# Performance work log

Measured on AMD Instinct MI355X. Metric: run time of the kernel, lower is better.

The kernel has to match this reference:

```python
import jax, jax.numpy as jnp
import numpy as np

K_F = 3
NUM = K_F * K_F - 1          # 8 non-center neighbors
IDX_REF = NUM // 2           # 4 (center insertion index)
PROP_TIME = 18
AFFINITY_GAMMA = 0.5
B, H, W = 4, 480, 640


def _bilinear(img, y, x):
    """Bilinear sample img [H,W] at float coords y,x [K,H,W]; zero outside."""
    Hh, Ww = img.shape
    y0 = jnp.floor(y)
    x0 = jnp.floor(x)

    def gather(yy, xx):
        valid = (yy >= 0) & (yy < Hh) & (xx >= 0) & (xx < Ww)
        yi = jnp.clip(yy.astype(jnp.int32), 0, Hh - 1)
        xi = jnp.clip(xx.astype(jnp.int32), 0, Ww - 1)
        return jnp.where(valid, img[yi, xi], 0.0)

    wy = y - y0
    wx = x - x0
    return ((1 - wy) * (1 - wx) * gather(y0, x0)
            + (1 - wy) * wx * gather(y0, x0 + 1)
            + wy * (1 - wx) * gather(y0 + 1, x0)
            + wy * wx * gather(y0 + 1, x0 + 1))


def _deform_prop(feat, dy, dx, aff):
    """Modulated deformable 3x3 conv with all-ones weight, zero bias, ch=1.
    feat [B,1,H,W]; dy,dx,aff [B,9,H,W]. Output = sum_k aff_k * sample_k."""
    b, _, h, w = feat.shape
    ky = jnp.array([-1, -1, -1, 0, 0, 0, 1, 1, 1], feat.dtype)
    kx = jnp.array([-1, 0, 1, -1, 0, 1, -1, 0, 1], feat.dtype)
    gy = jnp.arange(h, dtype=feat.dtype)[:, None]   # [H,1]
    gx = jnp.arange(w, dtype=feat.dtype)[None, :]   # [1,W]
    py = gy[None, None] + ky[None, :, None, None] + dy  # [B,9,H,W]
    px = gx[None, None] + kx[None, :, None, None] + dx
    samp = jax.vmap(_bilinear)(feat[:, 0], py, px)      # [B,9,H,W]
    return jnp.sum(samp * aff, axis=1, keepdims=True)


def _affinity_normalization(aff, scale):
    # TGASS: tanh / (gamma*num), abs-sum normalize (clamped at 1), reference = 1 - sum
    aff = jnp.tanh(aff) / (scale + 1e-8)
    s = jnp.sum(jnp.abs(aff), axis=1, keepdims=True) + 1e-4
    s = jnp.maximum(s, 1.0)
    aff = aff / s
    aff_ref = 1.0 - jnp.sum(aff, axis=1, keepdims=True)
    return jnp.concatenate([aff[:, :IDX_REF], aff_ref, aff[:, IDX_REF:]], axis=1)


def setup_inputs() -> dict:
    key = jax.random.key(0)
    k1, k2, k3, k4, k5 = jax.random.split(key, 5)
    feat_init = jax.random.uniform(k1, (B, 1, H, W), jnp.float32) * 10.0
    guidance = jax.random.normal(k2, (B, 24, H, W), jnp.float32)
    confidence = jax.random.uniform(k3, (B, 1, H, W), jnp.float32)
    dense = jax.random.uniform(k4, (B, 1, H, W), jnp.float32) * 10.0
    mask = (jax.random.uniform(k5, (B, 1, H, W)) < 0.05).astype(jnp.float32)
    feat_fix = dense * mask
    aff_scale_const = jnp.full((1,), AFFINITY_GAMMA * NUM, jnp.float32)
    return {"feat_init": feat_init, "guidance": guidance,
            "confidence": confidence, "feat_fix": feat_fix,
            "aff_scale_const": aff_scale_const}


def reference(feat_init, guidance, confidence, feat_fix, aff_scale_const):
    b = feat_init.shape[0]
    h, w = feat_init.shape[2], feat_init.shape[3]
    # offsets: chunk guidance into (o1, o2, aff), interleave, insert zero at center
    o1, o2, aff_g = jnp.split(guidance, 3, axis=1)
    off = jnp.concatenate([o1, o2], axis=1).reshape(b, NUM, 2, h, w)
    zc = jnp.zeros((b, 1, 2, h, w), off.dtype)
    off = jnp.concatenate([off[:, :IDX_REF], zc, off[:, IDX_REF:]], axis=1)
    dy, dx = off[:, :, 0], off[:, :, 1]          # [B,9,H,W]
    aff = _affinity_normalization(aff_g, aff_scale_const)

    # preserve_input: fixed-pixel mask (ch_f == 1)
    mask_fix = (feat_fix > 0.0).astype(feat_init.dtype)
    conf = (1.0 - mask_fix) * confidence + mask_fix
    feat = (1.0 - mask_fix) * feat_init + mask_fix * feat_fix

    def step(f, _):
        f = _deform_prop(f * conf, dy, dx, aff)
        f = (1.0 - mask_fix) * f + mask_fix * feat_fix
        return f, None

    feat, _ = jax.lax.scan(step, feat, None, length=PROP_TIME)
    return feat
```

## Files before the change

kernel.cpp:

```cpp
#include <hip/hip_runtime.h>
#include <hip/hip_fp16.h>
#include <hip/hip_cooperative_groups.h>

namespace cg = cooperative_groups;


#define HH 480
#define WW 640
#define BB 4
#define HWSZ (HH * WW)
#define NPIX (BB * HWSZ)
#define PROP_T 18
#define SLACK 704
#define NTHR 256
#define PXT 5
#define NBLK (NPIX / (NTHR * PXT))

struct f2u { float x, y; };

__device__ __forceinline__ float fast_tanh(float x) {
    x = fminf(fmaxf(x, -15.0f), 15.0f);
    float e = __expf(2.0f * x);
    return __fdividef(e - 1.0f, e + 1.0f);
}

__device__ __forceinline__ float affinities(const float* gb, float inv_scale,
                                            float t[8]) {
    float ssum = 1e-4f;
#pragma unroll
    for (int j = 0; j < 8; ++j) {
        float v = fast_tanh(gb[(16 + j) * HWSZ]) * inv_scale;
        t[j] = v; ssum += fabsf(v);
    }
    ssum = fmaxf(ssum, 1.0f);
    float rs = __fdividef(1.0f, ssum);
    float asum = 0.0f;
#pragma unroll
    for (int j = 0; j < 8; ++j) { t[j] *= rs; asum += t[j]; }
    return 1.0f - asum;
}

__device__ __forceinline__ void make_desc(int y, int x, int k,
                                          float dy, float dx, float ak,
                                          unsigned& pk, unsigned short& akh) {
    float py = (float)(y + k / 3 - 1) + dy;
    float px = (float)(x + k % 3 - 1) + dx;
    float y0f = floorf(py), x0f = floorf(px);
    float wy = py - y0f, wx = px - x0f;
    int y0 = (int)y0f, x0 = (int)x0f;
    if (y0 == -1)                 { ak *= wy;        wy = 1.0f; }
    else if (y0 == HH - 1)        { ak *= 1.0f - wy; wy = 0.0f; }
    else if (y0 < -1 || y0 >= HH) { ak = 0.0f; }
    if (x0 == -1)                 { ak *= wx;        wx = 1.0f; }
    else if (x0 == WW - 1)        { ak *= 1.0f - wx; wx = 0.0f; }
    else if (x0 < -1 || x0 >= WW) { ak = 0.0f; }
    int rel;
    if (ak == 0.0f) {
        rel = 0; wy = 0.0f; wx = 0.0f;
    } else {
        int yc = min(max(y0, -1), HH - 1);
        int xc = min(max(x0, -1), WW - 1);
        rel = (yc - y) * WW + (xc - x);
        rel = min(max(rel, -32767), 32767);
    }
    unsigned uy = (unsigned)(int)(wy * 255.0f + 0.5f);
    unsigned ux = (unsigned)(int)(wx * 255.0f + 0.5f);
    pk  = ((unsigned)(unsigned short)(short)rel << 16) | (uy << 8) | ux;
    akh = __half_as_ushort(__float2half(ak));
}

__device__ __forceinline__ float sample_rel(const float* __restrict__ fp,
                                            unsigned pk, unsigned short akh,
                                            float acc) {
    int rel = (int)(short)(pk >> 16);
    float wy = (float)((pk >> 8) & 0xffu) * (1.0f / 255.0f);
    float wx = (float)(pk & 0xffu) * (1.0f / 255.0f);
    float ak = __half2float(__ushort_as_half(akh));
    const float* p = fp + rel;
    f2u r0 = *reinterpret_cast<const f2u*>(p);
    f2u r1 = *reinterpret_cast<const f2u*>(p + WW);
    float bot = ak * wy;
    float top = ak - bot;
    float omwx = 1.0f - wx;
    acc = fmaf(top * omwx, r0.x, acc);
    acc = fmaf(top * wx,   r0.y, acc);
    acc = fmaf(bot * omwx, r1.x, acc);
    acc = fmaf(bot * wx,   r1.y, acc);
    return acc;
}

__global__ __launch_bounds__(NTHR) void precompute_kernel(
    const float* __restrict__ feat_init,
    const float* __restrict__ guid,
    const float* __restrict__ confidence,
    const float* __restrict__ feat_fix,
    const float* __restrict__ aff_scale,
    float* __restrict__ g0,
    unsigned* __restrict__ pk1Arr,
    unsigned short* __restrict__ akArr,
    unsigned* __restrict__ cfArr,
    float* __restrict__ ffpArr) {
    const int pix = blockIdx.x * NTHR + threadIdx.x;
    const int b = pix / HWSZ;
    const int q = pix - b * HWSZ;
    const int y = q / WW;
    const int x = q - y * WW;
    const float* gb = guid + (size_t)b * 24 * HWSZ + q;

    float ff = feat_fix[pix];
    float m  = (ff > 0.0f) ? 1.0f : 0.0f;
    float km = 1.0f - m;
    float conf = km * confidence[pix] + m;
    float f0   = km * feat_init[pix] + m * ff;
    g0[pix] = f0 * conf;
    ffpArr[pix] = m * ff;

    const float inv_scale = __fdividef(1.0f, aff_scale[0] + 1e-8f);
    float t[8];
    float aref = affinities(gb, inv_scale, t);
    cfArr[pix] = ((unsigned)__half_as_ushort(__float2half(aref)) << 16)
               | (unsigned)__half_as_ushort(__float2half(conf));

    unsigned pk[8];
    unsigned short akh[8];
#pragma unroll
    for (int n = 0; n < 8; ++n) {
        const int k = (n < 4) ? n : (n + 1);
        float dy = gb[(2 * n) * HWSZ];
        float dx = gb[(2 * n + 1) * HWSZ];
        make_desc(y, x, k, dy, dx, t[n], pk[n], akh[n]);
    }
    uint4* pd = reinterpret_cast<uint4*>(pk1Arr) + 2 * pix;
    pd[0] = make_uint4(pk[0], pk[1], pk[2], pk[3]);
    pd[1] = make_uint4(pk[4], pk[5], pk[6], pk[7]);
    uint4 kv;
    kv.x = (unsigned)akh[0] | ((unsigned)akh[1] << 16);
    kv.y = (unsigned)akh[2] | ((unsigned)akh[3] << 16);
    kv.z = (unsigned)akh[4] | ((unsigned)akh[5] << 16);
    kv.w = (unsigned)akh[6] | ((unsigned)akh[7] << 16);
    reinterpret_cast<uint4*>(akArr)[pix] = kv;
}

__global__ __launch_bounds__(NTHR, 4) void persist_kernel(
    const unsigned* __restrict__ pk1Arr,
    const unsigned short* __restrict__ akArr,
    const unsigned* __restrict__ cfArr,
    const float* __restrict__ ffpArr,
    float* __restrict__ fA,
    float* __restrict__ fB,
    float* __restrict__ out)
{
    cg::grid_group grid = cg::this_grid();
    const int base = blockIdx.x * (NTHR * PXT) + threadIdx.x;

    uint4 pka[PXT], pkb[PXT], akv[PXT];
    unsigned cfr[PXT];
    float    ffr[PXT];

#pragma unroll
    for (int i = 0; i < PXT; ++i) {
        const int pix = base + i * NTHR;
        const uint4* pd = reinterpret_cast<const uint4*>(pk1Arr) + 2 * pix;
        pka[i] = pd[0];
        pkb[i] = pd[1];
        akv[i] = reinterpret_cast<const uint4*>(akArr)[pix];
        cfr[i] = cfArr[pix];
        ffr[i] = ffpArr[pix];
    }

#pragma unroll 1
    for (int t = 0; t < PROP_T; ++t) {
        grid.sync();
        const float* fin = (t & 1) ? fB : fA;
        float* fout = (t == PROP_T - 1) ? out : ((t & 1) ? fA : fB);
        const bool last = (t == PROP_T - 1);
#pragma unroll
        for (int i = 0; i < PXT; ++i) {
            const int pix = base + i * NTHR;
            const float* fp = fin + pix;
            unsigned c = cfr[i];
            float aref = __half2float(__ushort_as_half((unsigned short)(c >> 16)));
            float conf = __half2float(__ushort_as_half((unsigned short)(c & 0xffffu)));
            float acc = aref * fp[0];
            uint4 A = pka[i], B = pkb[i], K = akv[i];
            acc = sample_rel(fp, A.x, (unsigned short)(K.x & 0xffffu), acc);
            acc = sample_rel(fp, A.y, (unsigned short)(K.x >> 16),     acc);
            acc = sample_rel(fp, A.z, (unsigned short)(K.y & 0xffffu), acc);
            acc = sample_rel(fp, A.w, (unsigned short)(K.y >> 16),     acc);
            acc = sample_rel(fp, B.x, (unsigned short)(K.z & 0xffffu), acc);
            acc = sample_rel(fp, B.y, (unsigned short)(K.z >> 16),     acc);
            acc = sample_rel(fp, B.z, (unsigned short)(K.w & 0xffffu), acc);
            acc = sample_rel(fp, B.w, (unsigned short)(K.w >> 16),     acc);
            float km = (ffr[i] > 0.0f) ? 0.0f : 1.0f;
            float fnew = fmaf(km, acc, ffr[i]);
            fout[pix] = last ? fnew : conf * fnew;
        }
    }
}

__global__ __launch_bounds__(NTHR) void step_kernel(
    const float* __restrict__ fin,
    float* __restrict__ fout,
    const unsigned* __restrict__ pk1Arr,
    const unsigned short* __restrict__ akArr,
    const unsigned* __restrict__ cfArr,
    const float* __restrict__ ffpArr,
    int last) {
    const int pix = blockIdx.x * NTHR + threadIdx.x;
    const float* fp = fin + pix;
    const uint4* pd = reinterpret_cast<const uint4*>(pk1Arr) + 2 * pix;
    uint4 A = pd[0], B = pd[1];
    uint4 K = reinterpret_cast<const uint4*>(akArr)[pix];
    unsigned c = cfArr[pix];
    float ffv = ffpArr[pix];
    float aref = __half2float(__ushort_as_half((unsigned short)(c >> 16)));
    float conf = __half2float(__ushort_as_half((unsigned short)(c & 0xffffu)));
    float acc = aref * fp[0];
    acc = sample_rel(fp, A.x, (unsigned short)(K.x & 0xffffu), acc);
    acc = sample_rel(fp, A.y, (unsigned short)(K.x >> 16),     acc);
    acc = sample_rel(fp, A.z, (unsigned short)(K.y & 0xffffu), acc);
    acc = sample_rel(fp, A.w, (unsigned short)(K.y >> 16),     acc);
    acc = sample_rel(fp, B.x, (unsigned short)(K.z & 0xffffu), acc);
    acc = sample_rel(fp, B.y, (unsigned short)(K.z >> 16),     acc);
    acc = sample_rel(fp, B.z, (unsigned short)(K.w & 0xffffu), acc);
    acc = sample_rel(fp, B.w, (unsigned short)(K.w >> 16),     acc);
    float km = (ffv > 0.0f) ? 0.0f : 1.0f;
    float fnew = fmaf(km, acc, ffv);
    fout[pix] = last ? fnew : conf * fnew;
}

extern "C" void kernel_launch(void* const* d_in, const int* in_sizes, int n_in,
                              void* d_out, int out_size, void* d_ws, size_t ws_size,
                              hipStream_t stream) {
    const float* feat_init  = (const float*)d_in[0];
    const float* guidance   = (const float*)d_in[1];
    const float* confidence = (const float*)d_in[2];
    const float* feat_fix   = (const float*)d_in[3];
    const float* aff_scale  = (const float*)d_in[4];

    const size_t bufFloats = (size_t)NPIX + 2 * SLACK;
    float* bufA = (float*)d_ws;
    float* bufB = bufA + bufFloats;
    unsigned* pk1Arr = (unsigned*)(bufB + bufFloats);
    unsigned short* akArr = (unsigned short*)(pk1Arr + 8 * (size_t)NPIX);
    unsigned* cfArr = (unsigned*)(akArr + 8 * (size_t)NPIX);
    float* ffpArr = (float*)(cfArr + NPIX);
    float* fA = bufA + SLACK;
    float* fB = bufB + SLACK;
    float* outp = (float*)d_out;

    hipMemsetAsync(bufA, 0, SLACK * sizeof(float), stream);
    hipMemsetAsync(bufA + SLACK + NPIX, 0, SLACK * sizeof(float), stream);
    hipMemsetAsync(bufB, 0, SLACK * sizeof(float), stream);
    hipMemsetAsync(bufB + SLACK + NPIX, 0, SLACK * sizeof(float), stream);

    precompute_kernel<<<NPIX / NTHR, NTHR, 0, stream>>>(
        feat_init, guidance, confidence, feat_fix, aff_scale,
        fA, pk1Arr, akArr, cfArr, ffpArr);

    bool tryCoop = false;
    {
        hipFuncAttributes fa{};
        if (hipFuncGetAttributes(&fa, reinterpret_cast<const void*>(persist_kernel))
                == hipSuccess && fa.localSizeBytes == 0) {
            int occ = 0;
            if (hipOccupancyMaxActiveBlocksPerMultiprocessor(
                    &occ, reinterpret_cast<const void*>(persist_kernel), NTHR, 0)
                    == hipSuccess) {
                int dev = 0, cu = 0;
                hipGetDevice(&dev);
                hipDeviceGetAttribute(&cu, hipDeviceAttributeMultiprocessorCount, dev);
                if ((long)occ * cu >= NBLK) tryCoop = true;
            }
        }
    }
    if (tryCoop) {
        void* args[] = { (void*)&pk1Arr, (void*)&akArr, (void*)&cfArr,
                         (void*)&ffpArr, (void*)&fA, (void*)&fB, (void*)&outp };
        if (hipLaunchCooperativeKernel(reinterpret_cast<void*>(persist_kernel),
                                       dim3(NBLK), dim3(NTHR), args, 0, stream)
                == hipSuccess)
            return;
    }

    for (int t = 0; t < PROP_T; ++t) {
        const float* fin = (t & 1) ? fB : fA;
        float* fout = (t == PROP_T - 1) ? outp : ((t & 1) ? fA : fB);
        step_kernel<<<NPIX / NTHR, NTHR, 0, stream>>>(
            fin, fout, pk1Arr, akArr, cfArr, ffpArr, (t == PROP_T - 1) ? 1 : 0);
    }
}
```

Before: 648.0 us.

## Replace cooperative grid.sync with custom atomic counter barrier in persistent kernel

Drops the cooperative-groups launch and grid.sync in favour of a normal launch plus a hand-rolled global barrier: block thread 0 atomically increments a monotonically growing counter and spins with s_sleep until all blocks have arrived. The barrier now runs only between steps, not before the first one. The separate fixed-value array is packed with the conf/aref word into a uint2 so each pixel needs one fewer load. Sched barriers are also inserted to split the sampling code into scheduling regions. The risk is that a non-cooperative launch does not guarantee all blocks are co-resident, which could deadlock if occupancy is lower than computed.

```diff
diff --git a/kernel.cpp b/kernel.cpp
--- a/kernel.cpp
+++ b/kernel.cpp
@@ -1,8 +1,5 @@
 #include <hip/hip_runtime.h>
 #include <hip/hip_fp16.h>
-#include <hip/hip_cooperative_groups.h>
-
-namespace cg = cooperative_groups;
 
 
 #define HH 480
@@ -98,8 +95,7 @@
     float* __restrict__ g0,
     unsigned* __restrict__ pk1Arr,
     unsigned short* __restrict__ akArr,
-    unsigned* __restrict__ cfArr,
-    float* __restrict__ ffpArr) {
+    uint2* __restrict__ cfArr) {
     const int pix = blockIdx.x * NTHR + threadIdx.x;
     const int b = pix / HWSZ;
     const int q = pix - b * HWSZ;
@@ -113,13 +109,16 @@
     float conf = km * confidence[pix] + m;
     float f0   = km * feat_init[pix] + m * ff;
     g0[pix] = f0 * conf;
-    ffpArr[pix] = m * ff;
 
     const float inv_scale = __fdividef(1.0f, aff_scale[0] + 1e-8f);
     float t[8];
     float aref = affinities(gb, inv_scale, t);
-    cfArr[pix] = ((unsigned)__half_as_ushort(__float2half(aref)) << 16)
-               | (unsigned)__half_as_ushort(__float2half(conf));
+    uint2 cf;
+    cf.x = ((unsigned)__half_as_ushort(__float2half(aref)) << 16)
+         | (unsigned)__half_as_ushort(__float2half(conf));
+    float mff = m * ff;
+    cf.y = __float_as_uint(mff);
+    cfArr[pix] = cf;
 
     unsigned pk[8];
     unsigned short akh[8];
@@ -144,18 +143,16 @@
 __global__ __launch_bounds__(NTHR, 4) void persist_kernel(
     const unsigned* __restrict__ pk1Arr,
     const unsigned short* __restrict__ akArr,
-    const unsigned* __restrict__ cfArr,
-    const float* __restrict__ ffpArr,
+    const uint2* __restrict__ cfArr,
     float* __restrict__ fA,
     float* __restrict__ fB,
-    float* __restrict__ out)
+    float* __restrict__ out,
+    int* __restrict__ bar)
 {
-    cg::grid_group grid = cg::this_grid();
     const int base = blockIdx.x * (NTHR * PXT) + threadIdx.x;
 
     uint4 pka[PXT], pkb[PXT], akv[PXT];
-    unsigned cfr[PXT];
-    float    ffr[PXT];
+    uint2 cfr[PXT];
 
 #pragma unroll
     for (int i = 0; i < PXT; ++i) {
@@ -165,12 +162,10 @@
         pkb[i] = pd[1];
         akv[i] = reinterpret_cast<const uint4*>(akArr)[pix];
         cfr[i] = cfArr[pix];
-        ffr[i] = ffpArr[pix];
     }
 
 #pragma unroll 1
     for (int t = 0; t < PROP_T; ++t) {
-        grid.sync();
         const float* fin = (t & 1) ? fB : fA;
         float* fout = (t == PROP_T - 1) ? out : ((t & 1) ? fA : fB);
         const bool last = (t == PROP_T - 1);
@@ -178,7 +173,7 @@
         for (int i = 0; i < PXT; ++i) {
             const int pix = base + i * NTHR;
             const float* fp = fin + pix;
-            unsigned c = cfr[i];
+            unsigned c = cfr[i].x;
             float aref = __half2float(__ushort_as_half((unsigned short)(c >> 16)));
             float conf = __half2float(__ushort_as_half((unsigned short)(c & 0xffffu)));
             float acc = aref * fp[0];
@@ -187,13 +182,31 @@
             acc = sample_rel(fp, A.y, (unsigned short)(K.x >> 16),     acc);
             acc = sample_rel(fp, A.z, (unsigned short)(K.y & 0xffffu), acc);
             acc = sample_rel(fp, A.w, (unsigned short)(K.y >> 16),     acc);
+            __builtin_amdgcn_sched_barrier(0);
             acc = sample_rel(fp, B.x, (unsigned short)(K.z & 0xffffu), acc);
             acc = sample_rel(fp, B.y, (unsigned short)(K.z >> 16),     acc);
             acc = sample_rel(fp, B.z, (unsigned short)(K.w & 0xffffu), acc);
             acc = sample_rel(fp, B.w, (unsigned short)(K.w >> 16),     acc);
-            float km = (ffr[i] > 0.0f) ? 0.0f : 1.0f;
-            float fnew = fmaf(km, acc, ffr[i]);
+            float mff = __uint_as_float(cfr[i].y);
+            float km = (mff > 0.0f) ? 0.0f : 1.0f;
+            float fnew = fmaf(km, acc, mff);
             fout[pix] = last ? fnew : conf * fnew;
+            __builtin_amdgcn_sched_barrier(0);
+        }
+
+        if (!last) {
+            __syncthreads();
+            if (threadIdx.x == 0) {
+                __threadfence();
+                atomicAdd(bar, 1);
+                const int target = (t + 1) * NBLK;
+                while (__hip_atomic_load(bar, __ATOMIC_ACQUIRE,
+                                         __HIP_MEMORY_SCOPE_AGENT) < target) {
+                    __builtin_amdgcn_s_sleep(4);
+                }
+                __threadfence();
+            }
+            __syncthreads();
         }
     }
 }
@@ -203,18 +216,16 @@
     float* __restrict__ fout,
     const unsigned* __restrict__ pk1Arr,
     const unsigned short* __restrict__ akArr,
-    const unsigned* __restrict__ cfArr,
-    const float* __restrict__ ffpArr,
+    const uint2* __restrict__ cfArr,
     int last) {
     const int pix = blockIdx.x * NTHR + threadIdx.x;
     const float* fp = fin + pix;
     const uint4* pd = reinterpret_cast<const uint4*>(pk1Arr) + 2 * pix;
     uint4 A = pd[0], B = pd[1];
     uint4 K = reinterpret_cast<const uint4*>(akArr)[pix];
-    unsigned c = cfArr[pix];
-    float ffv = ffpArr[pix];
-    float aref = __half2float(__ushort_as_half((unsigned short)(c >> 16)));
-    float conf = __half2float(__ushort_as_half((unsigned short)(c & 0xffffu)));
+    uint2 c2 = cfArr[pix];
+    float aref = __half2float(__ushort_as_half((unsigned short)(c2.x >> 16)));
+    float conf = __half2float(__ushort_as_half((unsigned short)(c2.x & 0xffffu)));
     float acc = aref * fp[0];
     acc = sample_rel(fp, A.x, (unsigned short)(K.x & 0xffffu), acc);
     acc = sample_rel(fp, A.y, (unsigned short)(K.x >> 16),     acc);
@@ -224,8 +235,9 @@
     acc = sample_rel(fp, B.y, (unsigned short)(K.z >> 16),     acc);
     acc = sample_rel(fp, B.z, (unsigned short)(K.w & 0xffffu), acc);
     acc = sample_rel(fp, B.w, (unsigned short)(K.w >> 16),     acc);
-    float km = (ffv > 0.0f) ? 0.0f : 1.0f;
-    float fnew = fmaf(km, acc, ffv);
+    float mff = __uint_as_float(c2.y);
+    float km = (mff > 0.0f) ? 0.0f : 1.0f;
+    float fnew = fmaf(km, acc, mff);
     fout[pix] = last ? fnew : conf * fnew;
 }
 
@@ -243,8 +255,8 @@
     float* bufB = bufA + bufFloats;
     unsigned* pk1Arr = (unsigned*)(bufB + bufFloats);
     unsigned short* akArr = (unsigned short*)(pk1Arr + 8 * (size_t)NPIX);
-    unsigned* cfArr = (unsigned*)(akArr + 8 * (size_t)NPIX);
-    float* ffpArr = (float*)(cfArr + NPIX);
+    uint2* cfArr = (uint2*)(akArr + 8 * (size_t)NPIX);
+    int* barPtr = (int*)(cfArr + NPIX);
     float* fA = bufA + SLACK;
     float* fB = bufB + SLACK;
     float* outp = (float*)d_out;
@@ -253,12 +265,13 @@
     hipMemsetAsync(bufA + SLACK + NPIX, 0, SLACK * sizeof(float), stream);
     hipMemsetAsync(bufB, 0, SLACK * sizeof(float), stream);
     hipMemsetAsync(bufB + SLACK + NPIX, 0, SLACK * sizeof(float), stream);
+    hipMemsetAsync(barPtr, 0, 128, stream);
 
     precompute_kernel<<<NPIX / NTHR, NTHR, 0, stream>>>(
         feat_init, guidance, confidence, feat_fix, aff_scale,
-        fA, pk1Arr, akArr, cfArr, ffpArr);
-
-    bool tryCoop = false;
+        fA, pk1Arr, akArr, cfArr);
+
+    bool usePersist = false;
     {
         hipFuncAttributes fa{};
         if (hipFuncGetAttributes(&fa, reinterpret_cast<const void*>(persist_kernel))
@@ -270,23 +283,20 @@
                 int dev = 0, cu = 0;
                 hipGetDevice(&dev);
                 hipDeviceGetAttribute(&cu, hipDeviceAttributeMultiprocessorCount, dev);
-                if ((long)occ * cu >= NBLK) tryCoop = true;
+                if ((long)occ * cu >= NBLK) usePersist = true;
             }
         }
     }
-    if (tryCoop) {
-        void* args[] = { (void*)&pk1Arr, (void*)&akArr, (void*)&cfArr,
-                         (void*)&ffpArr, (void*)&fA, (void*)&fB, (void*)&outp };
-        if (hipLaunchCooperativeKernel(reinterpret_cast<void*>(persist_kernel),
-                                       dim3(NBLK), dim3(NTHR), args, 0, stream)
-                == hipSuccess)
-            return;
+    if (usePersist) {
+        persist_kernel<<<NBLK, NTHR, 0, stream>>>(
+            pk1Arr, akArr, cfArr, fA, fB, outp, barPtr);
+        return;
     }
 
     for (int t = 0; t < PROP_T; ++t) {
         const float* fin = (t & 1) ? fB : fA;
         float* fout = (t == PROP_T - 1) ? outp : ((t & 1) ? fA : fB);
         step_kernel<<<NPIX / NTHR, NTHR, 0, stream>>>(
-            fin, fout, pk1Arr, akArr, cfArr, ffpArr, (t == PROP_T - 1) ? 1 : 0);
-    }
-}
+            fin, fout, pk1Arr, akArr, cfArr, (t == PROP_T - 1) ? 1 : 0);
+    }
+}
```

Result: no change. 657.3 us (+1.4%).
